# Kernel optimization log

Hardware: AMD Instinct MI355X
Metric: run time of the kernel (lower is better)

Reference implementation:

```python
import jax, jax.numpy as jnp
import numpy as np

B, T, D = 4, 50, 512
SRC, SENTS, WORDS = 400, 16, 40
NEG = jnp.float32(-1e30)  # stands in for -inf mask fill (numerically identical post-softmax)


def _seq_mask(lengths, max_len):
    # [n, max_len] bool, True where position < length
    return jnp.arange(max_len)[None, :] < lengths[:, None]


def _mlp_score(q, h, Wq, bq, Uc, v):
    # Bahdanau additive score: v^T tanh(W q + U h)
    # q: [b,t,d], h: [b,s,d] -> [b,t,s]
    wq = q @ Wq + bq                       # [b,t,d]
    uh = h @ Uc                            # [b,s,d]
    wquh = jnp.tanh(wq[:, :, None, :] + uh[:, None, :, :])  # [b,t,s,d]
    return jnp.einsum('btsd,d->bts', wquh, v)


def setup_inputs() -> dict:
    key = jax.random.key(0)
    ks = jax.random.split(key, 20)
    s = np.float32(1.0 / np.sqrt(D))
    def p(k, shape):
        return jax.random.normal(k, shape, jnp.float32) * s
    return {
        'source': jax.random.normal(ks[0], (B, T, D), jnp.float32),
        'src_bank': jax.random.normal(ks[1], (SRC, B, D), jnp.float32),
        'src_lengths': jax.random.randint(ks[2], (B,), 1, SRC + 1),
        'qa_sent_bank': jax.random.normal(ks[3], (SENTS, B, D), jnp.float32),
        'qa_sent_lengths': jax.random.randint(ks[4], (B,), 1, SENTS + 1),
        'qa_word_bank': jax.random.normal(ks[5], (WORDS, B, SENTS, D), jnp.float32),
        'qa_word_lengths': jax.random.randint(ks[6], (B, SENTS), 1, WORDS + 1),
        'Wq_word': p(ks[7], (D, D)), 'bq_word': jnp.zeros((D,), jnp.float32),
        'Uc_word': p(ks[8], (D, D)), 'v_word': p(ks[9], (D,)),
        'Wq_sent': p(ks[10], (D, D)), 'bq_sent': jnp.zeros((D,), jnp.float32),
        'Uc_sent': p(ks[11], (D, D)), 'v_sent': p(ks[12], (D,)),
        'Wq_pass': p(ks[13], (D, D)), 'bq_pass': jnp.zeros((D,), jnp.float32),
        'Uc_pass': p(ks[14], (D, D)), 'v_pass': p(ks[15], (D,)),
    }


def _forward(source, src_bank, qa_sent_bank, qa_word_bank,
             Wq_word, bq_word, Uc_word, v_word,
             Wq_sent, bq_sent, Uc_sent, v_sent,
             Wq_pass, bq_pass, Uc_pass, v_pass,
             src_lengths, qa_word_lengths):
    b = source.shape[0]
    # [words,b,sents,d] -> [b,sents,words,d] -> [b, sents*words, d]
    qa_word = jnp.transpose(qa_word_bank, (1, 2, 0, 3)).reshape(b, SENTS * WORDS, D)
    src = jnp.transpose(src_bank, (1, 0, 2))       # [b,src,d]
    sent = jnp.transpose(qa_sent_bank, (1, 0, 2))  # [b,sents,d]

    qa_word_align = _mlp_score(source, qa_word, Wq_word, bq_word, Uc_word, v_word)  # [b,t,sents*words]
    src_align = _mlp_score(source, src, Wq_pass, bq_pass, Uc_pass, v_pass)          # [b,t,src]
    qa_sent_align = _mlp_score(source, sent, Wq_sent, bq_sent, Uc_sent, v_sent)     # [b,t,sents]

    # hierarchical combination: word score scaled by its sentence score
    qa_hier = (qa_word_align.reshape(b, T, SENTS, WORDS)
               * qa_sent_align[..., None]).reshape(b, T, SENTS * WORDS)

    align = jnp.concatenate([src_align, qa_hier], axis=-1)  # [b,t,src+sents*words]

    qa_mask = _seq_mask(qa_word_lengths.reshape(-1), WORDS).reshape(b, SENTS * WORDS)[:, None, :]
    src_mask = _seq_mask(src_lengths, SRC)[:, None, :]
    mask = jnp.concatenate([src_mask, qa_mask], axis=-1)

    align = jnp.where(mask, align, NEG)
    align_vectors = jax.nn.softmax(align, axis=-1)  # joint length-masked softmax

    memory = jnp.concatenate([src, qa_word], axis=1)          # [b, src+sents*words, d]
    c = jnp.einsum('bts,bsd->btd', align_vectors, memory)     # weighted context sum
    return c


def reference(source, src_bank, src_lengths, qa_sent_bank, qa_sent_lengths,
              qa_word_bank, qa_word_lengths,
              Wq_word, bq_word, Uc_word, v_word,
              Wq_sent, bq_sent, Uc_sent, v_sent,
              Wq_pass, bq_pass, Uc_pass, v_pass):
    # qa_sent_lengths is accepted but unused, matching the original forward()
    return _forward(source, src_bank, qa_sent_bank, qa_word_bank,
                    Wq_word, bq_word, Uc_word, v_word,
                    Wq_sent, bq_sent, Uc_sent, v_sent,
                    Wq_pass, bq_pass, Uc_pass, v_pass,
                    src_lengths, qa_word_lengths)
```

## Files before the change

kernel.cpp:

```cpp
#include <hip/hip_runtime.h>
#include <hip/hip_bf16.h>


#define B_    4
#define T_    50
#define D_    512
#define SRC_  400
#define SENTS_ 16
#define WORDS_ 40
#define NW_   640
#define NMEM_ 1040
#define NK_   1056
#define NJOB_ 1056

#define C2L2E 2.8853900817779268f

typedef unsigned short ushort_t;
using s8v = __attribute__((ext_vector_type(8))) short;
using f4v = __attribute__((ext_vector_type(4))) float;

#define OFF_WQ_WORD 0
#define OFF_WQ_SENT 102400
#define OFF_WQ_PASS 204800
#define OFF_UH_SRC  307200
#define OFF_UH_WORD 1126400
#define OFF_UH_SENT 2437120
#define OFF_SC_SRC  2469888
#define OFF_SC_WORD 2549888
#define OFF_SC_SENT 2677888
#define P_BYTE_OFF  10724352ull
#define MT_BYTE_OFF 11265024ull
#define WT_BYTE_OFF 15590400ull

__device__ __forceinline__ ushort_t f2b(float f) {
    __hip_bfloat16 h = __float2bfloat16(f);
    return *(ushort_t*)&h;
}

__global__ __launch_bounds__(256) void k0f_transpose(
    const float* __restrict__ w0, const float* __restrict__ w1,
    const float* __restrict__ w2, const float* __restrict__ w3,
    const float* __restrict__ w4, const float* __restrict__ w5,
    const float* __restrict__ src_bank, const float* __restrict__ qa_word_bank,
    ushort_t* __restrict__ wt, ushort_t* __restrict__ mt)
{
    __shared__ float tile[32][33];
    int z = blockIdx.z;
    int tx = threadIdx.x & 31, ty = threadIdx.x >> 5;
    if (z < 6) {
        if (blockIdx.x >= 16) return;
        const float* W;
        switch (z) {
            case 0: W = w0; break; case 1: W = w1; break; case 2: W = w2; break;
            case 3: W = w3; break; case 4: W = w4; break; default: W = w5; break;
        }
        ushort_t* Wt = wt + z * (D_ * D_);
        int n0 = blockIdx.x * 32, k0 = blockIdx.y * 32;
#pragma unroll
        for (int a = 0; a < 4; ++a)
            tile[ty + a * 8][tx] = W[(k0 + ty + a * 8) * D_ + n0 + tx];
        __syncthreads();
#pragma unroll
        for (int a = 0; a < 4; ++a)
            Wt[(n0 + ty + a * 8) * D_ + k0 + tx] = f2b(tile[tx][ty + a * 8]);
    } else {
        int b = z - 6;
        int s0 = blockIdx.x * 32, d0 = blockIdx.y * 32;
#pragma unroll
        for (int a = 0; a < 4; ++a) {
            int s = s0 + ty + a * 8;
            float val = 0.f;
            if (s < SRC_) {
                val = src_bank[(s * B_ + b) * D_ + d0 + tx];
            } else if (s < NMEM_) {
                int j = s - SRC_; int se = j / WORDS_; int wd = j - se * WORDS_;
                val = qa_word_bank[((wd * B_ + b) * SENTS_ + se) * D_ + d0 + tx];
            }
            tile[ty + a * 8][tx] = val;
        }
        __syncthreads();
        ushort_t* base = mt + (size_t)b * D_ * NK_;
#pragma unroll
        for (int a = 0; a < 4; ++a) {
            int d = d0 + ty + a * 8;
            base[(size_t)d * NK_ + s0 + tx] = f2b(tile[tx][ty + a * 8]);
        }
    }
}

__global__ __launch_bounds__(256) void k1_gemm(
    const float* __restrict__ source, const float* __restrict__ src_bank,
    const float* __restrict__ qa_sent_bank, const float* __restrict__ qa_word_bank,
    const ushort_t* __restrict__ wt,
    const float* __restrict__ bq_word, const float* __restrict__ bq_sent,
    const float* __restrict__ bq_pass,
    float* __restrict__ wsf)
{
    __shared__ short At[64 * 32];
    __shared__ short Bt[64 * 32];
    int z = blockIdx.z;
    int M, atype; const float* bias; float* C;
    switch (z) {
        case 0: M = 200;  atype = 0; bias = bq_word; C = wsf + OFF_WQ_WORD; break;
        case 1: M = 200;  atype = 0; bias = bq_sent; C = wsf + OFF_WQ_SENT; break;
        case 2: M = 200;  atype = 0; bias = bq_pass; C = wsf + OFF_WQ_PASS; break;
        case 3: M = 2560; atype = 1; bias = nullptr; C = wsf + OFF_UH_WORD; break;
        case 4: M = 1600; atype = 2; bias = nullptr; C = wsf + OFF_UH_SRC;  break;
        default: M = 64;  atype = 3; bias = nullptr; C = wsf + OFF_UH_SENT; break;
    }
    int m0 = blockIdx.y * 64;
    if (m0 >= M) return;
    int n0 = blockIdx.x * 64;
    const ushort_t* W = wt + z * (D_ * D_);

    int tid = threadIdx.x;
    int lane = tid & 63, wv = tid >> 6;
    int quad = lane >> 4, l16 = lane & 15;
    int sm = tid >> 2, koff = (tid & 3) * 8;

    const float* arow = nullptr;
    {
        int r = m0 + sm;
        if (r < M) {
            if (atype == 0) arow = source + r * D_;
            else if (atype == 1) { int b = r / NW_; int j = r - b * NW_;
                                   int se = j / WORDS_; int wd = j - se * WORDS_;
                                   arow = qa_word_bank + ((wd * B_ + b) * SENTS_ + se) * D_; }
            else if (atype == 2) { int b = r / SRC_; int j = r - b * SRC_;
                                   arow = src_bank + (j * B_ + b) * D_; }
            else                 { int b = r >> 4; int s2 = r & 15;
                                   arow = qa_sent_bank + (s2 * B_ + b) * D_; }
        }
    }
    const ushort_t* wrow = W + (n0 + sm) * D_;

    f4v acc[4] = { {0.f,0.f,0.f,0.f}, {0.f,0.f,0.f,0.f},
                   {0.f,0.f,0.f,0.f}, {0.f,0.f,0.f,0.f} };

    for (int kk = 0; kk < 16; ++kk) {
        int k0 = kk * 32;
        union { ushort_t u[8]; int4 v; } pk;
        if (arow) {
            float4 f0 = *(const float4*)(arow + k0 + koff);
            float4 f1 = *(const float4*)(arow + k0 + koff + 4);
            pk.u[0] = f2b(f0.x); pk.u[1] = f2b(f0.y);
            pk.u[2] = f2b(f0.z); pk.u[3] = f2b(f0.w);
            pk.u[4] = f2b(f1.x); pk.u[5] = f2b(f1.y);
            pk.u[6] = f2b(f1.z); pk.u[7] = f2b(f1.w);
        } else {
            pk.v = int4{0, 0, 0, 0};
        }
        int4 bv = *(const int4*)(wrow + k0 + koff);
        *(int4*)(At + sm * 32 + koff) = pk.v;
        *(int4*)(Bt + sm * 32 + koff) = bv;
        __syncthreads();
        s8v af = *(const s8v*)(At + (wv * 16 + l16) * 32 + quad * 8);
#pragma unroll
        for (int ng = 0; ng < 4; ++ng) {
            s8v bf = *(const s8v*)(Bt + (ng * 16 + l16) * 32 + quad * 8);
            acc[ng] = __builtin_amdgcn_mfma_f32_16x16x32_bf16(af, bf, acc[ng], 0, 0, 0);
        }
        __syncthreads();
    }
#pragma unroll
    for (int ng = 0; ng < 4; ++ng) {
        int col = n0 + ng * 16 + l16;
        float bb = bias ? bias[col] : 0.f;
#pragma unroll
        for (int rr = 0; rr < 4; ++rr) {
            int row = m0 + wv * 16 + quad * 4 + rr;
            if (row < M) C[row * D_ + col] = (acc[ng][rr] + bb) * C2L2E;
        }
    }
}

__global__ __launch_bounds__(256) void k2_scores(
    const float* __restrict__ v_word, const float* __restrict__ v_sent,
    const float* __restrict__ v_pass,
    const int* __restrict__ src_lengths, const int* __restrict__ qa_word_lengths,
    float* __restrict__ wsf)
{
    int lane = threadIdx.x & 63;
    int job2 = blockIdx.x * 4 + (threadIdx.x >> 6);
    int job = job2 >> 1, th = job2 & 1;
    int b = job / NJOB_, slot = job - b * NJOB_;
    const float* uh; const float* v; const float* wq; float* out; int ostride;
    if (slot < SRC_) {
        if (slot >= src_lengths[b]) return;
        uh = wsf + OFF_UH_SRC + (b * SRC_ + slot) * D_;
        v = v_pass; wq = wsf + OFF_WQ_PASS + b * T_ * D_;
        out = wsf + OFF_SC_SRC + b * T_ * SRC_ + slot; ostride = SRC_;
    } else if (slot < NMEM_) {
        int j = slot - SRC_;
        int se = j / WORDS_; int wd = j - se * WORDS_;
        if (wd >= qa_word_lengths[b * SENTS_ + se]) return;
        uh = wsf + OFF_UH_WORD + (b * NW_ + j) * D_;
        v = v_word; wq = wsf + OFF_WQ_WORD + b * T_ * D_;
        out = wsf + OFF_SC_WORD + b * T_ * NW_ + j; ostride = NW_;
    } else {
        int s2 = slot - NMEM_;
        uh = wsf + OFF_UH_SENT + (b * SENTS_ + s2) * D_;
        v = v_sent; wq = wsf + OFF_WQ_SENT + b * T_ * D_;
        out = wsf + OFF_SC_SENT + b * T_ * SENTS_ + s2; ostride = SENTS_;
    }
    int d0 = lane * 8;
    float4 u0 = *(const float4*)(uh + d0);
    float4 u1 = *(const float4*)(uh + d0 + 4);
    float uhr[8] = {u0.x, u0.y, u0.z, u0.w, u1.x, u1.y, u1.z, u1.w};
    float4 v0 = *(const float4*)(v + d0);
    float4 v1 = *(const float4*)(v + d0 + 4);
    float vr[8] = {v0.x, v0.y, v0.z, v0.w, v1.x, v1.y, v1.z, v1.w};

    float vs = ((vr[0] + vr[1]) + (vr[2] + vr[3])) + ((vr[4] + vr[5]) + (vr[6] + vr[7]));
#pragma unroll
    for (int off = 32; off > 0; off >>= 1) vs += __shfl_xor(vs, off, 64);

    const float* wqh = wq + th * 25 * D_;
    float acc[25];
#pragma unroll 1
    for (int c = 0; c < 5; ++c) {
#pragma unroll
        for (int u5 = 0; u5 < 5; ++u5) {
            int u = c * 5 + u5;
            const float* wr = wqh + u * D_ + d0;
            float4 w0 = *(const float4*)(wr);
            float4 w1 = *(const float4*)(wr + 4);
            float wrr[8] = {w0.x, w0.y, w0.z, w0.w, w1.x, w1.y, w1.z, w1.w};
            float a = 0.f;
#pragma unroll
            for (int j = 0; j < 8; ++j) {
                float e = __builtin_amdgcn_exp2f(wrr[j] + uhr[j]);
                float r = __builtin_amdgcn_rcpf(e + 1.f);
                a = fmaf(vr[j], r, a);
            }
            acc[u] = a;
        }
    }
#pragma unroll
    for (int off = 32; off > 0; off >>= 1) {
#pragma unroll
        for (int u = 0; u < 25; ++u)
            acc[u] += __shfl_xor(acc[u], off, 64);
    }
    if (lane == 0) {
#pragma unroll
        for (int u = 0; u < 25; ++u)
            out[(th * 25 + u) * ostride] = fmaf(-2.f, acc[u], vs);
    }
}

__global__ __launch_bounds__(256) void k3a_softmax(
    const int* __restrict__ src_lengths, const int* __restrict__ qa_word_lengths,
    const float* __restrict__ wsf, ushort_t* __restrict__ P)
{
    __shared__ float p[NMEM_];
    __shared__ float red[4];
    int tid = threadIdx.x, lane = tid & 63, wv = tid >> 6;
    int bt = blockIdx.x, b = bt / T_, t = bt - b * T_;
    const float* sc_src  = wsf + OFF_SC_SRC  + bt * SRC_;
    const float* sc_word = wsf + OFF_SC_WORD + bt * NW_;
    const float* sc_sent = wsf + OFF_SC_SENT + bt * SENTS_;
    int slen = src_lengths[b];
    float mx = -3.0e38f;
    for (int j = tid; j < NMEM_; j += 256) {
        float val;
        if (j < SRC_) {
            val = (j < slen) ? sc_src[j] : -1e30f;
        } else {
            int jj = j - SRC_; int se = jj / WORDS_; int wd = jj - se * WORDS_;
            float raw = sc_word[jj] * sc_sent[se];
            val = (wd < qa_word_lengths[b * SENTS_ + se]) ? raw : -1e30f;
        }
        p[j] = val;
        mx = fmaxf(mx, val);
    }
#pragma unroll
    for (int off = 32; off > 0; off >>= 1) mx = fmaxf(mx, __shfl_xor(mx, off, 64));
    if (lane == 0) red[wv] = mx;
    __syncthreads();
    mx = fmaxf(fmaxf(red[0], red[1]), fmaxf(red[2], red[3]));
    __syncthreads();
    float lsum = 0.f;
    for (int j = tid; j < NMEM_; j += 256) {
        float e = __expf(p[j] - mx);
        p[j] = e; lsum += e;
    }
#pragma unroll
    for (int off = 32; off > 0; off >>= 1) lsum += __shfl_xor(lsum, off, 64);
    if (lane == 0) red[wv] = lsum;
    __syncthreads();
    float inv = 1.f / (red[0] + red[1] + red[2] + red[3]);
    ushort_t* prow = P + (size_t)(b * 64 + t) * NK_;
    for (int j = tid; j < NK_; j += 256)
        prow[j] = (j < NMEM_) ? f2b(p[j] * inv) : (ushort_t)0;
}

__global__ __launch_bounds__(256) void k3c_gemm(
    const ushort_t* __restrict__ P, const ushort_t* __restrict__ Mt,
    float* __restrict__ out)
{
    __shared__ short At[64 * 32];
    __shared__ short Bt[32 * 32];
    int b = blockIdx.y;
    int n0 = blockIdx.x * 32;
    int tid = threadIdx.x;
    int lane = tid & 63, wv = tid >> 6;
    int quad = lane >> 4, l16 = lane & 15;
    int smA = tid >> 2, koffA = (tid & 3) * 8;
    int smB = tid >> 3, koffB = (tid & 7) * 4;

    const ushort_t* arow = P + (size_t)(b * 64 + smA) * NK_ + koffA;
    const ushort_t* brow = Mt + ((size_t)(b * D_ + n0 + smB)) * NK_ + koffB;

    f4v acc[2] = { {0.f,0.f,0.f,0.f}, {0.f,0.f,0.f,0.f} };

    for (int kk = 0; kk < 33; ++kk) {
        int k0 = kk * 32;
        int4 av = *(const int4*)(arow + k0);
        int2 bv = *(const int2*)(brow + k0);
        *(int4*)(At + smA * 32 + koffA) = av;
        *(int2*)(Bt + smB * 32 + koffB) = bv;
        __syncthreads();
        s8v af = *(const s8v*)(At + (wv * 16 + l16) * 32 + quad * 8);
#pragma unroll
        for (int ng = 0; ng < 2; ++ng) {
            s8v bf = *(const s8v*)(Bt + (ng * 16 + l16) * 32 + quad * 8);
            acc[ng] = __builtin_amdgcn_mfma_f32_16x16x32_bf16(af, bf, acc[ng], 0, 0, 0);
        }
        __syncthreads();
    }
#pragma unroll
    for (int ng = 0; ng < 2; ++ng) {
        int col = n0 + ng * 16 + l16;
#pragma unroll
        for (int rr = 0; rr < 4; ++rr) {
            int row = wv * 16 + quad * 4 + rr;
            if (row < T_) out[(size_t)(b * T_ + row) * D_ + col] = acc[ng][rr];
        }
    }
}

extern "C" void kernel_launch(void* const* d_in, const int* in_sizes, int n_in,
                              void* d_out, int out_size, void* d_ws, size_t ws_size,
                              hipStream_t stream)
{
    (void)in_sizes; (void)n_in; (void)out_size; (void)ws_size;
    const float* source          = (const float*)d_in[0];
    const float* src_bank        = (const float*)d_in[1];
    const int*   src_lengths     = (const int*)d_in[2];
    const float* qa_sent_bank    = (const float*)d_in[3];
    const float* qa_word_bank    = (const float*)d_in[5];
    const int*   qa_word_lengths = (const int*)d_in[6];
    const float* Wq_word = (const float*)d_in[7];
    const float* bq_word = (const float*)d_in[8];
    const float* Uc_word = (const float*)d_in[9];
    const float* v_word  = (const float*)d_in[10];
    const float* Wq_sent = (const float*)d_in[11];
    const float* bq_sent = (const float*)d_in[12];
    const float* Uc_sent = (const float*)d_in[13];
    const float* v_sent  = (const float*)d_in[14];
    const float* Wq_pass = (const float*)d_in[15];
    const float* bq_pass = (const float*)d_in[16];
    const float* Uc_pass = (const float*)d_in[17];
    const float* v_pass  = (const float*)d_in[18];

    float* wsf = (float*)d_ws;
    ushort_t* Pb  = (ushort_t*)((char*)d_ws + P_BYTE_OFF);
    ushort_t* mt  = (ushort_t*)((char*)d_ws + MT_BYTE_OFF);
    ushort_t* wt  = (ushort_t*)((char*)d_ws + WT_BYTE_OFF);
    float* out = (float*)d_out;

    k0f_transpose<<<dim3(33, 16, 10), dim3(256), 0, stream>>>(
        Wq_word, Wq_sent, Wq_pass, Uc_word, Uc_pass, Uc_sent,
        src_bank, qa_word_bank, wt, mt);
    k1_gemm<<<dim3(8, 40, 6), dim3(256), 0, stream>>>(
        source, src_bank, qa_sent_bank, qa_word_bank, wt,
        bq_word, bq_sent, bq_pass, wsf);
    k2_scores<<<dim3(NJOB_ * 2), dim3(256), 0, stream>>>(
        v_word, v_sent, v_pass, src_lengths, qa_word_lengths, wsf);
    k3a_softmax<<<dim3(200), dim3(256), 0, stream>>>(src_lengths, qa_word_lengths, wsf, Pb);
    k3c_gemm<<<dim3(16, 4), dim3(256), 0, stream>>>(Pb, mt, out);
}
```

Baseline: 166.3 us.

## Fuse weight/memory transposes into GEMMs and split score jobs across four waves

```diff
diff --git a/kernel.cpp b/kernel.cpp
--- a/kernel.cpp
+++ b/kernel.cpp
@@ -29,94 +29,45 @@
 #define OFF_SC_WORD 2549888
 #define OFF_SC_SENT 2677888
 #define P_BYTE_OFF  10724352ull
-#define MT_BYTE_OFF 11265024ull
-#define WT_BYTE_OFF 15590400ull
 
 __device__ __forceinline__ ushort_t f2b(float f) {
     __hip_bfloat16 h = __float2bfloat16(f);
     return *(ushort_t*)&h;
 }
 
-__global__ __launch_bounds__(256) void k0f_transpose(
+__global__ __launch_bounds__(256) void k1_gemm(
+    const float* __restrict__ source, const float* __restrict__ src_bank,
+    const float* __restrict__ qa_sent_bank, const float* __restrict__ qa_word_bank,
     const float* __restrict__ w0, const float* __restrict__ w1,
     const float* __restrict__ w2, const float* __restrict__ w3,
     const float* __restrict__ w4, const float* __restrict__ w5,
-    const float* __restrict__ src_bank, const float* __restrict__ qa_word_bank,
-    ushort_t* __restrict__ wt, ushort_t* __restrict__ mt)
-{
-    __shared__ float tile[32][33];
-    int z = blockIdx.z;
-    int tx = threadIdx.x & 31, ty = threadIdx.x >> 5;
-    if (z < 6) {
-        if (blockIdx.x >= 16) return;
-        const float* W;
-        switch (z) {
-            case 0: W = w0; break; case 1: W = w1; break; case 2: W = w2; break;
-            case 3: W = w3; break; case 4: W = w4; break; default: W = w5; break;
-        }
-        ushort_t* Wt = wt + z * (D_ * D_);
-        int n0 = blockIdx.x * 32, k0 = blockIdx.y * 32;
-#pragma unroll
-        for (int a = 0; a < 4; ++a)
-            tile[ty + a * 8][tx] = W[(k0 + ty + a * 8) * D_ + n0 + tx];
-        __syncthreads();
-#pragma unroll
-        for (int a = 0; a < 4; ++a)
-            Wt[(n0 + ty + a * 8) * D_ + k0 + tx] = f2b(tile[tx][ty + a * 8]);
-    } else {
-        int b = z - 6;
-        int s0 = blockIdx.x * 32, d0 = blockIdx.y * 32;
-#pragma unroll
-        for (int a = 0; a < 4; ++a) {
-            int s = s0 + ty + a * 8;
-            float val = 0.f;
-            if (s < SRC_) {
-                val = src_bank[(s * B_ + b) * D_ + d0 + tx];
-            } else if (s < NMEM_) {
-                int j = s - SRC_; int se = j / WORDS_; int wd = j - se * WORDS_;
-                val = qa_word_bank[((wd * B_ + b) * SENTS_ + se) * D_ + d0 + tx];
-            }
-            tile[ty + a * 8][tx] = val;
-        }
-        __syncthreads();
-        ushort_t* base = mt + (size_t)b * D_ * NK_;
-#pragma unroll
-        for (int a = 0; a < 4; ++a) {
-            int d = d0 + ty + a * 8;
-            base[(size_t)d * NK_ + s0 + tx] = f2b(tile[tx][ty + a * 8]);
-        }
-    }
-}
-
-__global__ __launch_bounds__(256) void k1_gemm(
-    const float* __restrict__ source, const float* __restrict__ src_bank,
-    const float* __restrict__ qa_sent_bank, const float* __restrict__ qa_word_bank,
-    const ushort_t* __restrict__ wt,
     const float* __restrict__ bq_word, const float* __restrict__ bq_sent,
     const float* __restrict__ bq_pass,
     float* __restrict__ wsf)
 {
+    __shared__ float ftile[32][65];
     __shared__ short At[64 * 32];
     __shared__ short Bt[64 * 32];
     int z = blockIdx.z;
-    int M, atype; const float* bias; float* C;
+    int M, atype; const float* bias; float* C; const float* W;
     switch (z) {
-        case 0: M = 200;  atype = 0; bias = bq_word; C = wsf + OFF_WQ_WORD; break;
-        case 1: M = 200;  atype = 0; bias = bq_sent; C = wsf + OFF_WQ_SENT; break;
-        case 2: M = 200;  atype = 0; bias = bq_pass; C = wsf + OFF_WQ_PASS; break;
-        case 3: M = 2560; atype = 1; bias = nullptr; C = wsf + OFF_UH_WORD; break;
-        case 4: M = 1600; atype = 2; bias = nullptr; C = wsf + OFF_UH_SRC;  break;
-        default: M = 64;  atype = 3; bias = nullptr; C = wsf + OFF_UH_SENT; break;
+        case 0: M = 200;  atype = 0; bias = bq_word; C = wsf + OFF_WQ_WORD; W = w0; break;
+        case 1: M = 200;  atype = 0; bias = bq_sent; C = wsf + OFF_WQ_SENT; W = w1; break;
+        case 2: M = 200;  atype = 0; bias = bq_pass; C = wsf + OFF_WQ_PASS; W = w2; break;
+        case 3: M = 2560; atype = 1; bias = nullptr; C = wsf + OFF_UH_WORD; W = w3; break;
+        case 4: M = 1600; atype = 2; bias = nullptr; C = wsf + OFF_UH_SRC;  W = w4; break;
+        default: M = 64;  atype = 3; bias = nullptr; C = wsf + OFF_UH_SENT; W = w5; break;
     }
     int m0 = blockIdx.y * 64;
     if (m0 >= M) return;
     int n0 = blockIdx.x * 64;
-    const ushort_t* W = wt + z * (D_ * D_);
 
     int tid = threadIdx.x;
     int lane = tid & 63, wv = tid >> 6;
     int quad = lane >> 4, l16 = lane & 15;
     int sm = tid >> 2, koff = (tid & 3) * 8;
+    int wr = tid >> 3, wc = (tid & 7) * 8;
+    int tn = tid >> 2, tk = (tid & 3) * 8;
 
     const float* arow = nullptr;
     {
@@ -132,7 +83,6 @@
                                    arow = qa_sent_bank + (s2 * B_ + b) * D_; }
         }
     }
-    const ushort_t* wrow = W + (n0 + sm) * D_;
 
     f4v acc[4] = { {0.f,0.f,0.f,0.f}, {0.f,0.f,0.f,0.f},
                    {0.f,0.f,0.f,0.f}, {0.f,0.f,0.f,0.f} };
@@ -150,9 +100,17 @@
         } else {
             pk.v = int4{0, 0, 0, 0};
         }
-        int4 bv = *(const int4*)(wrow + k0 + koff);
+        const float* wsrc = W + (size_t)(k0 + wr) * D_ + n0 + wc;
+        float4 g0 = *(const float4*)(wsrc);
+        float4 g1 = *(const float4*)(wsrc + 4);
         *(int4*)(At + sm * 32 + koff) = pk.v;
-        *(int4*)(Bt + sm * 32 + koff) = bv;
+        *(float4*)(&ftile[wr][wc]) = g0;
+        *(float4*)(&ftile[wr][wc + 4]) = g1;
+        __syncthreads();
+        union { ushort_t u[8]; int4 v; } tb;
+#pragma unroll
+        for (int i = 0; i < 8; ++i) tb.u[i] = f2b(ftile[tk + i][tn]);
+        *(int4*)(Bt + tn * 32 + tk) = tb.v;
         __syncthreads();
         s8v af = *(const s8v*)(At + (wv * 16 + l16) * 32 + quad * 8);
 #pragma unroll
@@ -171,6 +129,42 @@
             int row = m0 + wv * 16 + quad * 4 + rr;
             if (row < M) C[row * D_ + col] = (acc[ng][rr] + bb) * C2L2E;
         }
+    }
+}
+
+template<int NT>
+__device__ __forceinline__ void score_chunk(
+    const float* __restrict__ wq, int tb, int ostride, int lane,
+    const float uhr[8], const float vr[8], float vs,
+    float* __restrict__ sco)
+{
+    int d0 = lane * 8;
+    float acc[NT];
+#pragma unroll
+    for (int u = 0; u < NT; ++u) {
+        const float* wr = wq + (tb + u) * D_ + d0;
+        float4 w0 = *(const float4*)(wr);
+        float4 w1 = *(const float4*)(wr + 4);
+        float wrr[8] = {w0.x, w0.y, w0.z, w0.w, w1.x, w1.y, w1.z, w1.w};
+        float a = 0.f;
+#pragma unroll
+        for (int j = 0; j < 8; ++j) {
+            float e = __builtin_amdgcn_exp2f(wrr[j] + uhr[j]);
+            float r = __builtin_amdgcn_rcpf(e + 1.f);
+            a = fmaf(vr[j], r, a);
+        }
+        acc[u] = a;
+    }
+#pragma unroll
+    for (int off = 32; off > 0; off >>= 1) {
+#pragma unroll
+        for (int u = 0; u < NT; ++u)
+            acc[u] += __shfl_xor(acc[u], off, 64);
+    }
+    if (lane == 0) {
+#pragma unroll
+        for (int u = 0; u < NT; ++u)
+            sco[(tb + u) * ostride] = fmaf(-2.f, acc[u], vs);
     }
 }
 
@@ -180,28 +174,27 @@
     const int* __restrict__ src_lengths, const int* __restrict__ qa_word_lengths,
     float* __restrict__ wsf)
 {
-    int lane = threadIdx.x & 63;
-    int job2 = blockIdx.x * 4 + (threadIdx.x >> 6);
-    int job = job2 >> 1, th = job2 & 1;
+    int lane = threadIdx.x & 63, th = threadIdx.x >> 6;
+    int job = blockIdx.x;
     int b = job / NJOB_, slot = job - b * NJOB_;
-    const float* uh; const float* v; const float* wq; float* out; int ostride;
+    const float* uh; const float* v; const float* wq; float* sco; int ostride;
     if (slot < SRC_) {
         if (slot >= src_lengths[b]) return;
         uh = wsf + OFF_UH_SRC + (b * SRC_ + slot) * D_;
         v = v_pass; wq = wsf + OFF_WQ_PASS + b * T_ * D_;
-        out = wsf + OFF_SC_SRC + b * T_ * SRC_ + slot; ostride = SRC_;
+        sco = wsf + OFF_SC_SRC + b * T_ * SRC_ + slot; ostride = SRC_;
     } else if (slot < NMEM_) {
         int j = slot - SRC_;
         int se = j / WORDS_; int wd = j - se * WORDS_;
         if (wd >= qa_word_lengths[b * SENTS_ + se]) return;
         uh = wsf + OFF_UH_WORD + (b * NW_ + j) * D_;
         v = v_word; wq = wsf + OFF_WQ_WORD + b * T_ * D_;
-        out = wsf + OFF_SC_WORD + b * T_ * NW_ + j; ostride = NW_;
+        sco = wsf + OFF_SC_WORD + b * T_ * NW_ + j; ostride = NW_;
     } else {
         int s2 = slot - NMEM_;
         uh = wsf + OFF_UH_SENT + (b * SENTS_ + s2) * D_;
         v = v_sent; wq = wsf + OFF_WQ_SENT + b * T_ * D_;
-        out = wsf + OFF_SC_SENT + b * T_ * SENTS_ + s2; ostride = SENTS_;
+        sco = wsf + OFF_SC_SENT + b * T_ * SENTS_ + s2; ostride = SENTS_;
     }
     int d0 = lane * 8;
     float4 u0 = *(const float4*)(uh + d0);
@@ -210,43 +203,14 @@
     float4 v0 = *(const float4*)(v + d0);
     float4 v1 = *(const float4*)(v + d0 + 4);
     float vr[8] = {v0.x, v0.y, v0.z, v0.w, v1.x, v1.y, v1.z, v1.w};
-
     float vs = ((vr[0] + vr[1]) + (vr[2] + vr[3])) + ((vr[4] + vr[5]) + (vr[6] + vr[7]));
 #pragma unroll
     for (int off = 32; off > 0; off >>= 1) vs += __shfl_xor(vs, off, 64);
 
-    const float* wqh = wq + th * 25 * D_;
-    float acc[25];
-#pragma unroll 1
-    for (int c = 0; c < 5; ++c) {
-#pragma unroll
-        for (int u5 = 0; u5 < 5; ++u5) {
-            int u = c * 5 + u5;
-            const float* wr = wqh + u * D_ + d0;
-            float4 w0 = *(const float4*)(wr);
-            float4 w1 = *(const float4*)(wr + 4);
-            float wrr[8] = {w0.x, w0.y, w0.z, w0.w, w1.x, w1.y, w1.z, w1.w};
-            float a = 0.f;
-#pragma unroll
-            for (int j = 0; j < 8; ++j) {
-                float e = __builtin_amdgcn_exp2f(wrr[j] + uhr[j]);
-                float r = __builtin_amdgcn_rcpf(e + 1.f);
-                a = fmaf(vr[j], r, a);
-            }
-            acc[u] = a;
-        }
-    }
-#pragma unroll
-    for (int off = 32; off > 0; off >>= 1) {
-#pragma unroll
-        for (int u = 0; u < 25; ++u)
-            acc[u] += __shfl_xor(acc[u], off, 64);
-    }
-    if (lane == 0) {
-#pragma unroll
-        for (int u = 0; u < 25; ++u)
-            out[(th * 25 + u) * ostride] = fmaf(-2.f, acc[u], vs);
-    }
+    if (th == 0)      score_chunk<13>(wq, 0,  ostride, lane, uhr, vr, vs, sco);
+    else if (th == 1) score_chunk<13>(wq, 13, ostride, lane, uhr, vr, vs, sco);
+    else if (th == 2) score_chunk<12>(wq, 26, ostride, lane, uhr, vr, vs, sco);
+    else              score_chunk<12>(wq, 38, ostride, lane, uhr, vr, vs, sco);
 }
 
 __global__ __launch_bounds__(256) void k3a_softmax(
@@ -296,9 +260,11 @@
 }
 
 __global__ __launch_bounds__(256) void k3c_gemm(
-    const ushort_t* __restrict__ P, const ushort_t* __restrict__ Mt,
+    const ushort_t* __restrict__ P,
+    const float* __restrict__ src_bank, const float* __restrict__ qa_word_bank,
     float* __restrict__ out)
 {
+    __shared__ float ftile[32][33];
     __shared__ short At[64 * 32];
     __shared__ short Bt[32 * 32];
     int b = blockIdx.y;
@@ -307,19 +273,31 @@
     int lane = tid & 63, wv = tid >> 6;
     int quad = lane >> 4, l16 = lane & 15;
     int smA = tid >> 2, koffA = (tid & 3) * 8;
-    int smB = tid >> 3, koffB = (tid & 7) * 4;
+    int br = tid >> 3, bc = (tid & 7) * 4;
+    int td = tid >> 3, ts = (tid & 7) * 4;
 
     const ushort_t* arow = P + (size_t)(b * 64 + smA) * NK_ + koffA;
-    const ushort_t* brow = Mt + ((size_t)(b * D_ + n0 + smB)) * NK_ + koffB;
 
     f4v acc[2] = { {0.f,0.f,0.f,0.f}, {0.f,0.f,0.f,0.f} };
 
     for (int kk = 0; kk < 33; ++kk) {
-        int k0 = kk * 32;
-        int4 av = *(const int4*)(arow + k0);
-        int2 bv = *(const int2*)(brow + k0);
+        int s0 = kk * 32;
+        int4 av = *(const int4*)(arow + s0);
+        int s = s0 + br;
+        float4 bv = {0.f, 0.f, 0.f, 0.f};
+        if (s < SRC_) {
+            bv = *(const float4*)(src_bank + (size_t)(s * B_ + b) * D_ + n0 + bc);
+        } else if (s < NMEM_) {
+            int jj = s - SRC_; int se = jj / WORDS_; int wd = jj - se * WORDS_;
+            bv = *(const float4*)(qa_word_bank + ((size_t)(wd * B_ + b) * SENTS_ + se) * D_ + n0 + bc);
+        }
         *(int4*)(At + smA * 32 + koffA) = av;
-        *(int2*)(Bt + smB * 32 + koffB) = bv;
+        *(float4*)(&ftile[br][bc]) = bv;
+        __syncthreads();
+        union { ushort_t u[4]; int2 v; } tb;
+#pragma unroll
+        for (int i = 0; i < 4; ++i) tb.u[i] = f2b(ftile[ts + i][td]);
+        *(int2*)(Bt + td * 32 + ts) = tb.v;
         __syncthreads();
         s8v af = *(const s8v*)(At + (wv * 16 + l16) * 32 + quad * 8);
 #pragma unroll
@@ -365,19 +343,15 @@
     const float* v_pass  = (const float*)d_in[18];
 
     float* wsf = (float*)d_ws;
-    ushort_t* Pb  = (ushort_t*)((char*)d_ws + P_BYTE_OFF);
-    ushort_t* mt  = (ushort_t*)((char*)d_ws + MT_BYTE_OFF);
-    ushort_t* wt  = (ushort_t*)((char*)d_ws + WT_BYTE_OFF);
+    ushort_t* Pb = (ushort_t*)((char*)d_ws + P_BYTE_OFF);
     float* out = (float*)d_out;
 
-    k0f_transpose<<<dim3(33, 16, 10), dim3(256), 0, stream>>>(
+    k1_gemm<<<dim3(8, 40, 6), dim3(256), 0, stream>>>(
+        source, src_bank, qa_sent_bank, qa_word_bank,
         Wq_word, Wq_sent, Wq_pass, Uc_word, Uc_pass, Uc_sent,
-        src_bank, qa_word_bank, wt, mt);
-    k1_gemm<<<dim3(8, 40, 6), dim3(256), 0, stream>>>(
-        source, src_bank, qa_sent_bank, qa_word_bank, wt,
         bq_word, bq_sent, bq_pass, wsf);
-    k2_scores<<<dim3(NJOB_ * 2), dim3(256), 0, stream>>>(
+    k2_scores<<<dim3(NJOB_ * B_), dim3(256), 0, stream>>>(
         v_word, v_sent, v_pass, src_lengths, qa_word_lengths, wsf);
     k3a_softmax<<<dim3(200), dim3(256), 0, stream>>>(src_lengths, qa_word_lengths, wsf, Pb);
-    k3c_gemm<<<dim3(16, 4), dim3(256), 0, stream>>>(Pb, mt, out);
-}
+    k3c_gemm<<<dim3(16, 4), dim3(256), 0, stream>>>(Pb, src_bank, qa_word_bank, out);
+}
```

Measured after the change: 168.7 us. No clear change (+1.5%).
